# Kernel optimization log

Measured on AMD Instinct MI355X. Metric: run time of the kernel, lower is better.

The kernel has to match this reference:

```python
import jax, jax.numpy as jnp
import numpy as np


def setup_inputs() -> dict:
    key = jax.random.key(0)
    ks = jax.random.split(key, 9)
    B, S, H = 4096, 64, 128
    scale = 0.05
    return {
        "feature_input": jax.random.normal(ks[0], (B, S, H), dtype=jnp.float32),
        "W1": jax.random.normal(ks[1], (S, H, H), dtype=jnp.float32) * scale,
        "b1": jax.random.normal(ks[2], (S, H), dtype=jnp.float32) * scale,
        "W3": jax.random.normal(ks[3], (S, H, H), dtype=jnp.float32) * scale,
        "b3": jax.random.normal(ks[4], (S, H), dtype=jnp.float32) * scale,
        "W_ih": jax.random.normal(ks[5], (3 * H, H), dtype=jnp.float32) * scale,
        "b_ih": jax.random.normal(ks[6], (3 * H,), dtype=jnp.float32) * scale,
        "W_hh": jax.random.normal(ks[7], (3 * H, H), dtype=jnp.float32) * scale,
        "b_hh": jax.random.normal(ks[8], (3 * H,), dtype=jnp.float32) * scale,
    }


def _gru_cell(x, h, W_ih, b_ih, W_hh, b_hh):
    # torch.nn.GRUCell math; gate order in weights is (r, z, n)
    gi = x @ W_ih.T + b_ih  # [N, 3H]
    gh = h @ W_hh.T + b_hh  # [N, 3H]
    H = h.shape[-1]
    gi_r, gi_z, gi_n = gi[:, :H], gi[:, H:2 * H], gi[:, 2 * H:]
    gh_r, gh_z, gh_n = gh[:, :H], gh[:, H:2 * H], gh[:, 2 * H:]
    r = jax.nn.sigmoid(gi_r + gh_r)
    z = jax.nn.sigmoid(gi_z + gh_z)
    n = jnp.tanh(gi_n + r * gh_n)
    return (1.0 - z) * n + z * h


def reference(feature_input, W1, b1, W3, b3, W_ih, b_ih, W_hh, b_hh):
    B, S, H = feature_input.shape
    # message pass: per-sen linear (batched over S as one einsum)
    state1 = jnp.einsum('bsh,soh->bso', feature_input, W1) + b1  # [B,S,H]
    # sum over sentences, broadcast-subtract own contribution
    state2 = jnp.sum(state1, axis=1, keepdims=True) - state1      # [B,S,H]
    state3 = jnp.einsum('bsh,soh->bso', state2, W3) + b3          # [B,S,H]
    # GRU cell update over flattened (B*S) nodes
    h_new = _gru_cell(state3.reshape(-1, H), feature_input.reshape(-1, H),
                      W_ih, b_ih, W_hh, b_hh)
    return feature_input + h_new.reshape(B, S, H)
```

## Files before the change

### kernel.cpp

```cpp
#include <hip/hip_runtime.h>
#include <stdint.h>

#define Bdim 4096
#define Sdim 64
#define Hdim 128

typedef __attribute__((ext_vector_type(8))) __bf16 bf16x8;
typedef __attribute__((ext_vector_type(4))) float f32x4;
typedef __attribute__((ext_vector_type(8))) unsigned short ushort8v;

__device__ __forceinline__ unsigned short f2bf(float f) {
  unsigned int u = __float_as_uint(f);
  u = u + 0x7fffu + ((u >> 16) & 1u);
  return (unsigned short)(u >> 16);
}
__device__ __forceinline__ float bf2f(unsigned short s) {
  return __uint_as_float(((unsigned int)s) << 16);
}
__device__ __forceinline__ float sigm(float x) { return 1.0f / (1.0f + __expf(-x)); }
__device__ __forceinline__ float fast_tanh(float x) {
  float t = __expf(-2.0f * fabsf(x));
  float y = (1.0f - t) / (1.0f + t);
  return copysignf(y, x);
}

__device__ __forceinline__ void glds16(const void* g, void* l) {
  auto* gp = reinterpret_cast<__attribute__((address_space(1))) unsigned int*>(
      reinterpret_cast<uintptr_t>(g));
  auto* lp = reinterpret_cast<__attribute__((address_space(3))) unsigned int*>(
      static_cast<uint32_t>(reinterpret_cast<uintptr_t>(l)));
  __builtin_amdgcn_global_load_lds(gp, lp, 16, 0, 0);
}

__device__ __forceinline__ void stage_w(unsigned short* Ws, const unsigned short* wsrc,
                                        int w, int lane) {
#pragma unroll
  for (int i = 0; i < 4; ++i) {
    int chunk = w * 4 + i;
    glds16(wsrc + (size_t)chunk * 512 + lane * 8, Ws + chunk * 512);
  }
}

__device__ __forceinline__ void stage_tile512(unsigned short* L, const float* __restrict__ src,
                                              int rsF, int t) {
#pragma unroll
  for (int it = 0; it < 4; ++it) {
    int c = t + it * 512;
    int r = c >> 4, bblk = c & 15;
    const float* p = src + (size_t)r * rsF + bblk * 8;
    float4 v0 = *(const float4*)p;
    float4 v1 = *(const float4*)(p + 4);
    ushort8v o;
    o[0] = f2bf(v0.x); o[1] = f2bf(v0.y); o[2] = f2bf(v0.z); o[3] = f2bf(v0.w);
    o[4] = f2bf(v1.x); o[5] = f2bf(v1.y); o[6] = f2bf(v1.z); o[7] = f2bf(v1.w);
    *(ushort8v*)(L + r * 128 + (bblk ^ (r & 15)) * 8) = o;
  }
}

__device__ __forceinline__ void mfma_gemm(f32x4 acc[8], const unsigned short* A,
                                          const unsigned short* Ws,
                                          const float* __restrict__ biasN,
                                          int w, int lane) {
  const int quad = lane >> 4, l15 = lane & 15;
  bf16x8 a[4];
#pragma unroll
  for (int k0 = 0; k0 < 4; ++k0)
    a[k0] = *(const bf16x8*)&A[(w * 16 + l15) * 128 + (((k0 << 2) | quad) ^ l15) * 8];
#pragma unroll
  for (int nt = 0; nt < 8; ++nt) {
    float b = biasN ? biasN[nt * 16 + l15] : 0.0f;
    f32x4 c = {b, b, b, b};
#pragma unroll
    for (int k0 = 0; k0 < 4; ++k0)
      c = __builtin_amdgcn_mfma_f32_16x16x32_bf16(
          a[k0], *(const bf16x8*)&Ws[((nt * 4 + k0) * 64 + lane) * 8], c, 0, 0, 0);
    acc[nt] = c;
  }
}

__global__ __launch_bounds__(256) void convert_kernel(
    const float* __restrict__ W1, const float* __restrict__ W3,
    const float* __restrict__ Wih, const float* __restrict__ Whh,
    const float* __restrict__ b1, unsigned short* __restrict__ wsW,
    float* __restrict__ b1s) {
  int cid = blockIdx.x * 256 + threadIdx.x;
  int mat = cid >> 11;
  int within = cid & 2047;
  int f = within >> 6, lane = within & 63;
  int nt = f >> 2, k0 = f & 3;
  int o = nt * 16 + (lane & 15);
  int hb = k0 * 32 + (lane >> 4) * 8;
  const float* src;
  if (mat < 64)       src = W1 + (size_t)mat * 16384;
  else if (mat < 128) src = W3 + (size_t)(mat - 64) * 16384;
  else if (mat < 131) src = Wih + (size_t)(mat - 128) * 16384;
  else                src = Whh + (size_t)(mat - 131) * 16384;
  const float* p = src + o * 128 + hb;
  float4 v0 = *(const float4*)p;
  float4 v1 = *(const float4*)(p + 4);
  ushort8v oo;
  oo[0] = f2bf(v0.x); oo[1] = f2bf(v0.y); oo[2] = f2bf(v0.z); oo[3] = f2bf(v0.w);
  oo[4] = f2bf(v1.x); oo[5] = f2bf(v1.y); oo[6] = f2bf(v1.z); oo[7] = f2bf(v1.w);
  *(ushort8v*)(wsW + (size_t)cid * 8) = oo;
  if (cid < 128) {
    float a = 0.0f;
    for (int s = 0; s < 64; ++s) a += b1[s * 128 + cid];
    b1s[cid] = a;
  }
}

__global__ __launch_bounds__(512) void sum_kernel(
    const float* __restrict__ X, const unsigned short* __restrict__ wsW1,
    float* __restrict__ sumP) {
  __shared__ unsigned short Xs[2][128 * 128];
  __shared__ unsigned short Ws[2][128 * 128];
  const int t = threadIdx.x;
  const int lane = t & 63, w = t >> 6, quad = lane >> 4, l15 = lane & 15;
  const int m0 = blockIdx.x * 128;
  const int sc = blockIdx.y;
  f32x4 acc[8] = {};

  stage_w(Ws[0], wsW1 + (size_t)(sc * 8) * 16384, w, lane);
  stage_tile512(Xs[0], X + (size_t)m0 * 8192 + (sc * 8) * 128, 8192, t);
  __syncthreads();

  for (int si = 0; si < 8; ++si) {
    const int cur = si & 1;
    float4 xr[4][2];
    if (si < 7) {
      int s = sc * 8 + si + 1;
      stage_w(Ws[cur ^ 1], wsW1 + (size_t)s * 16384, w, lane);
#pragma unroll
      for (int it = 0; it < 4; ++it) {
        int c = t + it * 512;
        int r = c >> 4, bblk = c & 15;
        const float* p = X + (size_t)(m0 + r) * 8192 + s * 128 + bblk * 8;
        xr[it][0] = *(const float4*)p;
        xr[it][1] = *(const float4*)(p + 4);
      }
    }
    {
      bf16x8 a[4];
#pragma unroll
      for (int k0 = 0; k0 < 4; ++k0)
        a[k0] = *(const bf16x8*)&Xs[cur][(w * 16 + l15) * 128 + (((k0 << 2) | quad) ^ l15) * 8];
#pragma unroll
      for (int nt = 0; nt < 8; ++nt)
#pragma unroll
        for (int k0 = 0; k0 < 4; ++k0)
          acc[nt] = __builtin_amdgcn_mfma_f32_16x16x32_bf16(
              a[k0], *(const bf16x8*)&Ws[cur][((nt * 4 + k0) * 64 + lane) * 8], acc[nt], 0, 0, 0);
    }
    if (si < 7) {
#pragma unroll
      for (int it = 0; it < 4; ++it) {
        int c = t + it * 512;
        int r = c >> 4, bblk = c & 15;
        ushort8v o;
        o[0] = f2bf(xr[it][0].x); o[1] = f2bf(xr[it][0].y);
        o[2] = f2bf(xr[it][0].z); o[3] = f2bf(xr[it][0].w);
        o[4] = f2bf(xr[it][1].x); o[5] = f2bf(xr[it][1].y);
        o[6] = f2bf(xr[it][1].z); o[7] = f2bf(xr[it][1].w);
        *(ushort8v*)(Xs[cur ^ 1] + r * 128 + (bblk ^ (r & 15)) * 8) = o;
      }
    }
    __syncthreads();
  }
  float* dst = sumP + (size_t)sc * 524288 + (size_t)(m0 + w * 16) * 128;
#pragma unroll
  for (int nt = 0; nt < 8; ++nt)
#pragma unroll
    for (int r = 0; r < 4; ++r)
      dst[(quad * 4 + r) * 128 + nt * 16 + l15] = acc[nt][r];
}

__global__ __launch_bounds__(256) void reduce_kernel(
    const float* __restrict__ sumP, const float* __restrict__ b1s,
    float* __restrict__ sumS) {
  int i = blockIdx.x * 256 + threadIdx.x;
  float4 acc = *(const float4*)(b1s + (i & 31) * 4);
#pragma unroll
  for (int c = 0; c < 8; ++c) {
    float4 v = *(const float4*)(sumP + (size_t)c * 524288 + (size_t)i * 4);
    acc.x += v.x; acc.y += v.y; acc.z += v.z; acc.w += v.w;
  }
  *(float4*)(sumS + (size_t)i * 4) = acc;
}

__global__ __launch_bounds__(512) void fused_kernel(
    const float* __restrict__ X, const unsigned short* __restrict__ wsW,
    const float* __restrict__ b1, const float* __restrict__ b3,
    const float* __restrict__ bih, const float* __restrict__ bhh,
    const float* __restrict__ sumS, float* __restrict__ out) {
  __shared__ unsigned short Xs[128 * 128];
  __shared__ unsigned short S2[128 * 128];
  __shared__ unsigned short Ws[2][128 * 128];
  const int t = threadIdx.x;
  const int lane = t & 63, w = t >> 6, quad = lane >> 4, l15 = lane & 15;
  const int m0 = blockIdx.x * 128;
  const int s = blockIdx.y;

  const unsigned short* Wptr[8] = {
      wsW + (size_t)s * 16384,
      wsW + (size_t)(64 + s) * 16384,
      wsW + (size_t)128 * 16384,
      wsW + (size_t)131 * 16384,
      wsW + (size_t)129 * 16384,
      wsW + (size_t)132 * 16384,
      wsW + (size_t)130 * 16384,
      wsW + (size_t)133 * 16384};

  stage_w(Ws[0], Wptr[0], w, lane);
  stage_tile512(Xs, X + (size_t)m0 * 8192 + s * 128, 8192, t);
  __syncthreads();

  f32x4 gi[8], gh[8];
  float rg[8][4], zg[8][4];

  stage_w(Ws[1], Wptr[1], w, lane);
  mfma_gemm(gi, Xs, Ws[0], b1 + s * 128, w, lane);
  {
    const float* sp = sumS + (size_t)(m0 + w * 16) * 128;
#pragma unroll
    for (int nt = 0; nt < 8; ++nt) {
      int n = nt * 16 + l15;
#pragma unroll
      for (int r = 0; r < 4; ++r) {
        int rr = quad * 4 + r;
        float v = sp[rr * 128 + n] - gi[nt][r];
        S2[(w * 16 + rr) * 128 + ((n >> 3) ^ rr) * 8 + (n & 7)] = f2bf(v);
      }
    }
  }
  __syncthreads();
  stage_w(Ws[0], Wptr[2], w, lane);
  mfma_gemm(gi, S2, Ws[1], b3 + s * 128, w, lane);
#pragma unroll
  for (int nt = 0; nt < 8; ++nt) {
    int n = nt * 16 + l15;
#pragma unroll
    for (int r = 0; r < 4; ++r) {
      int rr = quad * 4 + r;
      S2[(w * 16 + rr) * 128 + ((n >> 3) ^ rr) * 8 + (n & 7)] = f2bf(gi[nt][r]);
    }
  }
  __syncthreads();
  stage_w(Ws[1], Wptr[3], w, lane);
  mfma_gemm(gi, S2, Ws[0], bih + 0 * 128, w, lane);
  __syncthreads();
  stage_w(Ws[0], Wptr[4], w, lane);
  mfma_gemm(gh, Xs, Ws[1], bhh + 0 * 128, w, lane);
#pragma unroll
  for (int nt = 0; nt < 8; ++nt)
#pragma unroll
    for (int r = 0; r < 4; ++r) rg[nt][r] = sigm(gi[nt][r] + gh[nt][r]);
  __syncthreads();
  stage_w(Ws[1], Wptr[5], w, lane);
  mfma_gemm(gi, S2, Ws[0], bih + 1 * 128, w, lane);
  __syncthreads();
  stage_w(Ws[0], Wptr[6], w, lane);
  mfma_gemm(gh, Xs, Ws[1], bhh + 1 * 128, w, lane);
#pragma unroll
  for (int nt = 0; nt < 8; ++nt)
#pragma unroll
    for (int r = 0; r < 4; ++r) zg[nt][r] = sigm(gi[nt][r] + gh[nt][r]);
  __syncthreads();
  stage_w(Ws[1], Wptr[7], w, lane);
  mfma_gemm(gi, S2, Ws[0], bih + 2 * 128, w, lane);
  __syncthreads();
  mfma_gemm(gh, Xs, Ws[1], bhh + 2 * 128, w, lane);
  {
    float* op = out + ((size_t)(m0 + w * 16) * 64 + s) * 128;
#pragma unroll
    for (int nt = 0; nt < 8; ++nt) {
      int n = nt * 16 + l15;
#pragma unroll
      for (int r = 0; r < 4; ++r) {
        int rr = quad * 4 + r;
        float nv = fast_tanh(gi[nt][r] + rg[nt][r] * gh[nt][r]);
        float xv = bf2f(Xs[(w * 16 + rr) * 128 + ((n >> 3) ^ rr) * 8 + (n & 7)]);
        float hn = (1.0f - zg[nt][r]) * nv + zg[nt][r] * xv;
        op[(size_t)rr * 8192 + n] = xv + hn;
      }
    }
  }
}

extern "C" void kernel_launch(void* const* d_in, const int* in_sizes, int n_in,
                              void* d_out, int out_size, void* d_ws, size_t ws_size,
                              hipStream_t stream) {
  const float* X   = (const float*)d_in[0];
  const float* W1  = (const float*)d_in[1];
  const float* b1  = (const float*)d_in[2];
  const float* W3  = (const float*)d_in[3];
  const float* b3  = (const float*)d_in[4];
  const float* Wih = (const float*)d_in[5];
  const float* bih = (const float*)d_in[6];
  const float* Whh = (const float*)d_in[7];
  const float* bhh = (const float*)d_in[8];
  float* out = (float*)d_out;

  const size_t W_BYTES = (size_t)134 * 32768;
  unsigned short* wsW = (unsigned short*)d_ws;
  float* b1s  = (float*)((char*)d_ws + W_BYTES);
  float* sumS = (float*)((char*)d_ws + W_BYTES + 512);
  float* sumP = (float*)((char*)d_ws + W_BYTES + 512 + 2097152);

  convert_kernel<<<1072, 256, 0, stream>>>(W1, W3, Wih, Whh, b1, wsW, b1s);
  sum_kernel<<<dim3(32, 8), 512, 0, stream>>>(X, wsW, sumP);
  reduce_kernel<<<512, 256, 0, stream>>>(sumP, b1s, sumS);
  fused_kernel<<<dim3(32, 64), 512, 0, stream>>>(X, wsW, b1, b3, bih, bhh, sumS, out);
}
```

Before: 449.6 us.

## Use 16 waves per block with 2x2 MFMA sub-tiles per wave

```diff
diff --git a/kernel.cpp b/kernel.cpp
--- a/kernel.cpp
+++ b/kernel.cpp
@@ -22,6 +22,12 @@
   float t = __expf(-2.0f * fabsf(x));
   float y = (1.0f - t) / (1.0f + t);
   return copysignf(y, x);
+}
+__device__ __forceinline__ ushort8v pack8(float4 v0, float4 v1) {
+  ushort8v o;
+  o[0] = f2bf(v0.x); o[1] = f2bf(v0.y); o[2] = f2bf(v0.z); o[3] = f2bf(v0.w);
+  o[4] = f2bf(v1.x); o[5] = f2bf(v1.y); o[6] = f2bf(v1.z); o[7] = f2bf(v1.w);
+  return o;
 }
 
 __device__ __forceinline__ void glds16(const void* g, void* l) {
@@ -35,46 +41,39 @@
 __device__ __forceinline__ void stage_w(unsigned short* Ws, const unsigned short* wsrc,
                                         int w, int lane) {
 #pragma unroll
-  for (int i = 0; i < 4; ++i) {
-    int chunk = w * 4 + i;
+  for (int i = 0; i < 2; ++i) {
+    int chunk = w * 2 + i;
     glds16(wsrc + (size_t)chunk * 512 + lane * 8, Ws + chunk * 512);
   }
 }
 
-__device__ __forceinline__ void stage_tile512(unsigned short* L, const float* __restrict__ src,
-                                              int rsF, int t) {
-#pragma unroll
-  for (int it = 0; it < 4; ++it) {
-    int c = t + it * 512;
-    int r = c >> 4, bblk = c & 15;
-    const float* p = src + (size_t)r * rsF + bblk * 8;
-    float4 v0 = *(const float4*)p;
-    float4 v1 = *(const float4*)(p + 4);
-    ushort8v o;
-    o[0] = f2bf(v0.x); o[1] = f2bf(v0.y); o[2] = f2bf(v0.z); o[3] = f2bf(v0.w);
-    o[4] = f2bf(v1.x); o[5] = f2bf(v1.y); o[6] = f2bf(v1.z); o[7] = f2bf(v1.w);
-    *(ushort8v*)(L + r * 128 + (bblk ^ (r & 15)) * 8) = o;
-  }
-}
-
-__device__ __forceinline__ void mfma_gemm(f32x4 acc[8], const unsigned short* A,
-                                          const unsigned short* Ws,
-                                          const float* __restrict__ biasN,
-                                          int w, int lane) {
-  const int quad = lane >> 4, l15 = lane & 15;
-  bf16x8 a[4];
-#pragma unroll
-  for (int k0 = 0; k0 < 4; ++k0)
-    a[k0] = *(const bf16x8*)&A[(w * 16 + l15) * 128 + (((k0 << 2) | quad) ^ l15) * 8];
-#pragma unroll
-  for (int nt = 0; nt < 8; ++nt) {
-    float b = biasN ? biasN[nt * 16 + l15] : 0.0f;
-    f32x4 c = {b, b, b, b};
+__device__ __forceinline__ void gemm32(f32x4 acc[2][2], const unsigned short* A,
+                                       const unsigned short* W,
+                                       const float* __restrict__ biasN,
+                                       int wr, int wc, int quad, int l15) {
+  const int lane = quad * 16 + l15;
+  bf16x8 a[2][4];
+#pragma unroll
+  for (int rt = 0; rt < 2; ++rt) {
+    int row = wr * 32 + rt * 16 + l15;
 #pragma unroll
     for (int k0 = 0; k0 < 4; ++k0)
-      c = __builtin_amdgcn_mfma_f32_16x16x32_bf16(
-          a[k0], *(const bf16x8*)&Ws[((nt * 4 + k0) * 64 + lane) * 8], c, 0, 0, 0);
-    acc[nt] = c;
+      a[rt][k0] = *(const bf16x8*)&A[row * 128 + (((k0 << 2) | quad) ^ l15) * 8];
+  }
+#pragma unroll
+  for (int ntl = 0; ntl < 2; ++ntl) {
+    int nt = wc * 2 + ntl;
+    float b = biasN[nt * 16 + l15];
+    f32x4 c0 = {b, b, b, b};
+    f32x4 c1 = c0;
+#pragma unroll
+    for (int k0 = 0; k0 < 4; ++k0) {
+      bf16x8 bw = *(const bf16x8*)&W[((nt * 4 + k0) * 64 + lane) * 8];
+      c0 = __builtin_amdgcn_mfma_f32_16x16x32_bf16(a[0][k0], bw, c0, 0, 0, 0);
+      c1 = __builtin_amdgcn_mfma_f32_16x16x32_bf16(a[1][k0], bw, c1, 0, 0, 0);
+    }
+    acc[0][ntl] = c0;
+    acc[1][ntl] = c1;
   }
 }
 
@@ -98,10 +97,7 @@
   const float* p = src + o * 128 + hb;
   float4 v0 = *(const float4*)p;
   float4 v1 = *(const float4*)(p + 4);
-  ushort8v oo;
-  oo[0] = f2bf(v0.x); oo[1] = f2bf(v0.y); oo[2] = f2bf(v0.z); oo[3] = f2bf(v0.w);
-  oo[4] = f2bf(v1.x); oo[5] = f2bf(v1.y); oo[6] = f2bf(v1.z); oo[7] = f2bf(v1.w);
-  *(ushort8v*)(wsW + (size_t)cid * 8) = oo;
+  *(ushort8v*)(wsW + (size_t)cid * 8) = pack8(v0, v1);
   if (cid < 128) {
     float a = 0.0f;
     for (int s = 0; s < 64; ++s) a += b1[s * 128 + cid];
@@ -109,30 +105,39 @@
   }
 }
 
-__global__ __launch_bounds__(512) void sum_kernel(
+__global__ __launch_bounds__(1024) void sum_kernel(
     const float* __restrict__ X, const unsigned short* __restrict__ wsW1,
     float* __restrict__ sumP) {
   __shared__ unsigned short Xs[2][128 * 128];
   __shared__ unsigned short Ws[2][128 * 128];
   const int t = threadIdx.x;
   const int lane = t & 63, w = t >> 6, quad = lane >> 4, l15 = lane & 15;
+  const int wr = w >> 2, wc = w & 3;
   const int m0 = blockIdx.x * 128;
   const int sc = blockIdx.y;
-  f32x4 acc[8] = {};
+  f32x4 acc[2][2] = {};
 
   stage_w(Ws[0], wsW1 + (size_t)(sc * 8) * 16384, w, lane);
-  stage_tile512(Xs[0], X + (size_t)m0 * 8192 + (sc * 8) * 128, 8192, t);
+#pragma unroll
+  for (int it = 0; it < 2; ++it) {
+    int c = t + it * 1024;
+    int r = c >> 4, bblk = c & 15;
+    const float* p = X + (size_t)(m0 + r) * 8192 + (sc * 8) * 128 + bblk * 8;
+    float4 v0 = *(const float4*)p;
+    float4 v1 = *(const float4*)(p + 4);
+    *(ushort8v*)(Xs[0] + r * 128 + (bblk ^ (r & 15)) * 8) = pack8(v0, v1);
+  }
   __syncthreads();
 
   for (int si = 0; si < 8; ++si) {
     const int cur = si & 1;
-    float4 xr[4][2];
+    float4 xr[2][2];
     if (si < 7) {
       int s = sc * 8 + si + 1;
       stage_w(Ws[cur ^ 1], wsW1 + (size_t)s * 16384, w, lane);
 #pragma unroll
-      for (int it = 0; it < 4; ++it) {
-        int c = t + it * 512;
+      for (int it = 0; it < 2; ++it) {
+        int c = t + it * 1024;
         int r = c >> 4, bblk = c & 15;
         const float* p = X + (size_t)(m0 + r) * 8192 + s * 128 + bblk * 8;
         xr[it][0] = *(const float4*)p;
@@ -140,38 +145,46 @@
       }
     }
     {
-      bf16x8 a[4];
-#pragma unroll
-      for (int k0 = 0; k0 < 4; ++k0)
-        a[k0] = *(const bf16x8*)&Xs[cur][(w * 16 + l15) * 128 + (((k0 << 2) | quad) ^ l15) * 8];
-#pragma unroll
-      for (int nt = 0; nt < 8; ++nt)
+      bf16x8 a[2][4];
+#pragma unroll
+      for (int rt = 0; rt < 2; ++rt) {
+        int row = wr * 32 + rt * 16 + l15;
 #pragma unroll
         for (int k0 = 0; k0 < 4; ++k0)
-          acc[nt] = __builtin_amdgcn_mfma_f32_16x16x32_bf16(
-              a[k0], *(const bf16x8*)&Ws[cur][((nt * 4 + k0) * 64 + lane) * 8], acc[nt], 0, 0, 0);
+          a[rt][k0] = *(const bf16x8*)&Xs[cur][row * 128 + (((k0 << 2) | quad) ^ l15) * 8];
+      }
+#pragma unroll
+      for (int ntl = 0; ntl < 2; ++ntl) {
+        int nt = wc * 2 + ntl;
+#pragma unroll
+        for (int k0 = 0; k0 < 4; ++k0) {
+          bf16x8 bw = *(const bf16x8*)&Ws[cur][((nt * 4 + k0) * 64 + lane) * 8];
+          acc[0][ntl] = __builtin_amdgcn_mfma_f32_16x16x32_bf16(a[0][k0], bw, acc[0][ntl], 0, 0, 0);
+          acc[1][ntl] = __builtin_amdgcn_mfma_f32_16x16x32_bf16(a[1][k0], bw, acc[1][ntl], 0, 0, 0);
+        }
+      }
     }
     if (si < 7) {
 #pragma unroll
-      for (int it = 0; it < 4; ++it) {
-        int c = t + it * 512;
+      for (int it = 0; it < 2; ++it) {
+        int c = t + it * 1024;
         int r = c >> 4, bblk = c & 15;
-        ushort8v o;
-        o[0] = f2bf(xr[it][0].x); o[1] = f2bf(xr[it][0].y);
-        o[2] = f2bf(xr[it][0].z); o[3] = f2bf(xr[it][0].w);
-        o[4] = f2bf(xr[it][1].x); o[5] = f2bf(xr[it][1].y);
-        o[6] = f2bf(xr[it][1].z); o[7] = f2bf(xr[it][1].w);
-        *(ushort8v*)(Xs[cur ^ 1] + r * 128 + (bblk ^ (r & 15)) * 8) = o;
+        *(ushort8v*)(Xs[cur ^ 1] + r * 128 + (bblk ^ (r & 15)) * 8) = pack8(xr[it][0], xr[it][1]);
       }
     }
     __syncthreads();
   }
-  float* dst = sumP + (size_t)sc * 524288 + (size_t)(m0 + w * 16) * 128;
-#pragma unroll
-  for (int nt = 0; nt < 8; ++nt)
-#pragma unroll
-    for (int r = 0; r < 4; ++r)
-      dst[(quad * 4 + r) * 128 + nt * 16 + l15] = acc[nt][r];
+  float* dst = sumP + (size_t)sc * 524288 + (size_t)m0 * 128;
+#pragma unroll
+  for (int rt = 0; rt < 2; ++rt)
+#pragma unroll
+    for (int ntl = 0; ntl < 2; ++ntl)
+#pragma unroll
+      for (int r = 0; r < 4; ++r) {
+        int row = wr * 32 + rt * 16 + quad * 4 + r;
+        int n = (wc * 2 + ntl) * 16 + l15;
+        dst[(size_t)row * 128 + n] = acc[rt][ntl][r];
+      }
 }
 
 __global__ __launch_bounds__(256) void reduce_kernel(
@@ -187,7 +200,7 @@
   *(float4*)(sumS + (size_t)i * 4) = acc;
 }
 
-__global__ __launch_bounds__(512) void fused_kernel(
+__global__ __launch_bounds__(1024) void fused_kernel(
     const float* __restrict__ X, const unsigned short* __restrict__ wsW,
     const float* __restrict__ b1, const float* __restrict__ b3,
     const float* __restrict__ bih, const float* __restrict__ bhh,
@@ -197,6 +210,7 @@
   __shared__ unsigned short Ws[2][128 * 128];
   const int t = threadIdx.x;
   const int lane = t & 63, w = t >> 6, quad = lane >> 4, l15 = lane & 15;
+  const int wr = w >> 2, wc = w & 3;
   const int m0 = blockIdx.x * 128;
   const int s = blockIdx.y;
 
@@ -211,79 +225,97 @@
       wsW + (size_t)133 * 16384};
 
   stage_w(Ws[0], Wptr[0], w, lane);
-  stage_tile512(Xs, X + (size_t)m0 * 8192 + s * 128, 8192, t);
-  __syncthreads();
-
-  f32x4 gi[8], gh[8];
-  float rg[8][4], zg[8][4];
+#pragma unroll
+  for (int it = 0; it < 2; ++it) {
+    int c = t + it * 1024;
+    int r = c >> 4, bblk = c & 15;
+    const float* p = X + (size_t)(m0 + r) * 8192 + s * 128 + bblk * 8;
+    float4 v0 = *(const float4*)p;
+    float4 v1 = *(const float4*)(p + 4);
+    *(ushort8v*)(Xs + r * 128 + (bblk ^ (r & 15)) * 8) = pack8(v0, v1);
+  }
+  __syncthreads();
+
+  f32x4 gi[2][2], gh[2][2];
+  float rg[2][2][4], zg[2][2][4];
 
   stage_w(Ws[1], Wptr[1], w, lane);
-  mfma_gemm(gi, Xs, Ws[0], b1 + s * 128, w, lane);
+  gemm32(gi, Xs, Ws[0], b1 + s * 128, wr, wc, quad, l15);
   {
-    const float* sp = sumS + (size_t)(m0 + w * 16) * 128;
-#pragma unroll
-    for (int nt = 0; nt < 8; ++nt) {
-      int n = nt * 16 + l15;
+    const float* sp = sumS + (size_t)m0 * 128;
+#pragma unroll
+    for (int rt = 0; rt < 2; ++rt)
+#pragma unroll
+      for (int ntl = 0; ntl < 2; ++ntl)
+#pragma unroll
+        for (int r = 0; r < 4; ++r) {
+          int rr = quad * 4 + r;
+          int row = wr * 32 + rt * 16 + rr;
+          int n = (wc * 2 + ntl) * 16 + l15;
+          float v = sp[(size_t)row * 128 + n] - gi[rt][ntl][r];
+          S2[row * 128 + ((n >> 3) ^ rr) * 8 + (n & 7)] = f2bf(v);
+        }
+  }
+  __syncthreads();
+  stage_w(Ws[0], Wptr[2], w, lane);
+  gemm32(gi, S2, Ws[1], b3 + s * 128, wr, wc, quad, l15);
+  __syncthreads();
+#pragma unroll
+  for (int rt = 0; rt < 2; ++rt)
+#pragma unroll
+    for (int ntl = 0; ntl < 2; ++ntl)
 #pragma unroll
       for (int r = 0; r < 4; ++r) {
         int rr = quad * 4 + r;
-        float v = sp[rr * 128 + n] - gi[nt][r];
-        S2[(w * 16 + rr) * 128 + ((n >> 3) ^ rr) * 8 + (n & 7)] = f2bf(v);
-      }
-    }
-  }
-  __syncthreads();
-  stage_w(Ws[0], Wptr[2], w, lane);
-  mfma_gemm(gi, S2, Ws[1], b3 + s * 128, w, lane);
-#pragma unroll
-  for (int nt = 0; nt < 8; ++nt) {
-    int n = nt * 16 + l15;
-#pragma unroll
-    for (int r = 0; r < 4; ++r) {
-      int rr = quad * 4 + r;
-      S2[(w * 16 + rr) * 128 + ((n >> 3) ^ rr) * 8 + (n & 7)] = f2bf(gi[nt][r]);
-    }
-  }
+        int row = wr * 32 + rt * 16 + rr;
+        int n = (wc * 2 + ntl) * 16 + l15;
+        S2[row * 128 + ((n >> 3) ^ rr) * 8 + (n & 7)] = f2bf(gi[rt][ntl][r]);
+      }
   __syncthreads();
   stage_w(Ws[1], Wptr[3], w, lane);
-  mfma_gemm(gi, S2, Ws[0], bih + 0 * 128, w, lane);
+  gemm32(gi, S2, Ws[0], bih + 0 * 128, wr, wc, quad, l15);
   __syncthreads();
   stage_w(Ws[0], Wptr[4], w, lane);
-  mfma_gemm(gh, Xs, Ws[1], bhh + 0 * 128, w, lane);
-#pragma unroll
-  for (int nt = 0; nt < 8; ++nt)
-#pragma unroll
-    for (int r = 0; r < 4; ++r) rg[nt][r] = sigm(gi[nt][r] + gh[nt][r]);
+  gemm32(gh, Xs, Ws[1], bhh + 0 * 128, wr, wc, quad, l15);
+#pragma unroll
+  for (int rt = 0; rt < 2; ++rt)
+#pragma unroll
+    for (int ntl = 0; ntl < 2; ++ntl)
+#pragma unroll
+      for (int r = 0; r < 4; ++r)
+        rg[rt][ntl][r] = sigm(gi[rt][ntl][r] + gh[rt][ntl][r]);
   __syncthreads();
   stage_w(Ws[1], Wptr[5], w, lane);
-  mfma_gemm(gi, S2, Ws[0], bih + 1 * 128, w, lane);
+  gemm32(gi, S2, Ws[0], bih + 1 * 128, wr, wc, quad, l15);
   __syncthreads();
   stage_w(Ws[0], Wptr[6], w, lane);
-  mfma_gemm(gh, Xs, Ws[1], bhh + 1 * 128, w, lane);
-#pragma unroll
-  for (int nt = 0; nt < 8; ++nt)
-#pragma unroll
-    for (int r = 0; r < 4; ++r) zg[nt][r] = sigm(gi[nt][r] + gh[nt][r]);
+  gemm32(gh, Xs, Ws[1], bhh + 1 * 128, wr, wc, quad, l15);
+#pragma unroll
+  for (int rt = 0; rt < 2; ++rt)
+#pragma unroll
+    for (int ntl = 0; ntl < 2; ++ntl)
+#pragma unroll
+      for (int r = 0; r < 4; ++r)
+        zg[rt][ntl][r] = sigm(gi[rt][ntl][r] + gh[rt][ntl][r]);
   __syncthreads();
   stage_w(Ws[1], Wptr[7], w, lane);
-  mfma_gemm(gi, S2, Ws[0], bih + 2 * 128, w, lane);
-  __syncthreads();
-  mfma_gemm(gh, Xs, Ws[1], bhh + 2 * 128, w, lane);
-  {
-    float* op = out + ((size_t)(m0 + w * 16) * 64 + s) * 128;
-#pragma unroll
-    for (int nt = 0; nt < 8; ++nt) {
-      int n = nt * 16 + l15;
+  gemm32(gi, S2, Ws[0], bih + 2 * 128, wr, wc, quad, l15);
+  __syncthreads();
+  gemm32(gh, Xs, Ws[1], bhh + 2 * 128, wr, wc, quad, l15);
+#pragma unroll
+  for (int rt = 0; rt < 2; ++rt)
+#pragma unroll
+    for (int ntl = 0; ntl < 2; ++ntl)
 #pragma unroll
       for (int r = 0; r < 4; ++r) {
         int rr = quad * 4 + r;
-        float nv = fast_tanh(gi[nt][r] + rg[nt][r] * gh[nt][r]);
-        float xv = bf2f(Xs[(w * 16 + rr) * 128 + ((n >> 3) ^ rr) * 8 + (n & 7)]);
-        float hn = (1.0f - zg[nt][r]) * nv + zg[nt][r] * xv;
-        op[(size_t)rr * 8192 + n] = xv + hn;
-      }
-    }
-  }
+        int row = wr * 32 + rt * 16 + rr;
+        int n = (wc * 2 + ntl) * 16 + l15;
+        float nv = fast_tanh(gi[rt][ntl][r] + rg[rt][ntl][r] * gh[rt][ntl][r]);
+        float xv = bf2f(Xs[row * 128 + ((n >> 3) ^ rr) * 8 + (n & 7)]);
+        float hn = (1.0f - zg[rt][ntl][r]) * nv + zg[rt][ntl][r] * xv;
+        out[((size_t)(m0 + row) * 64 + s) * 128 + n] = xv + hn;
+      }
 }
 
 extern "C" void kernel_launch(void* const* d_in, const int* in_sizes, int n_in,
@@ -307,7 +339,7 @@
   float* sumP = (float*)((char*)d_ws + W_BYTES + 512 + 2097152);
 
   convert_kernel<<<1072, 256, 0, stream>>>(W1, W3, Wih, Whh, b1, wsW, b1s);
-  sum_kernel<<<dim3(32, 8), 512, 0, stream>>>(X, wsW, sumP);
+  sum_kernel<<<dim3(32, 8), 1024, 0, stream>>>(X, wsW, sumP);
   reduce_kernel<<<512, 256, 0, stream>>>(sumP, b1s, sumS);
-  fused_kernel<<<dim3(32, 64), 512, 0, stream>>>(X, wsW, b1, b3, bih, bhh, sumS, out);
-}
+  fused_kernel<<<dim3(32, 64), 1024, 0, stream>>>(X, wsW, b1, b3, bih, bhh, sumS, out);
+}
```

Measured after the change: 409.3 us. 1.1x faster.
